# Performance work log

Hardware: AMD Instinct MI355X
Metric: run time of the kernel (lower is better)

Reference implementation:

```python
import jax, jax.numpy as jnp
from jax import lax
import numpy as np

EMBED_HD = 3
DECODE_HD = 128
B, TX, TS = 256, 512, 512


def _lstm(x_seq, h0, c0, Wih, Whh, bih, bhh):
    """PyTorch-convention LSTM over time. x_seq: [T, B, D]; returns final h [B, H].
    Gate order i, f, g, o; gates = x W_ih^T + h W_hh^T + b_ih + b_hh."""
    b = bih + bhh

    def step(carry, x_t):
        h, c = carry
        gates = x_t @ Wih.T + h @ Whh.T + b  # [B, 4H]
        i, f, g, o = jnp.split(gates, 4, axis=-1)
        c = jax.nn.sigmoid(f) * c + jax.nn.sigmoid(i) * jnp.tanh(g)
        h = jax.nn.sigmoid(o) * jnp.tanh(c)
        return (h, c), None

    (hT, _cT), _ = lax.scan(step, (h0, c0), x_seq)
    return hT


def setup_inputs() -> dict:
    key = jax.random.key(0)
    ks = jax.random.split(key, 16)
    f32 = jnp.float32
    return {
        "x": jax.random.normal(ks[0], (B, TX, 8), f32),
        "s": jax.random.normal(ks[1], (B, TS, 6), f32),
        "h0": jax.random.normal(ks[2], (B, EMBED_HD), f32),
        "c0": jax.random.normal(ks[3], (B, EMBED_HD), f32),
        "We_ih": jax.random.normal(ks[4], (4 * EMBED_HD, 8), f32) * 0.1,
        "We_hh": jax.random.normal(ks[5], (4 * EMBED_HD, EMBED_HD), f32) * 0.1,
        "be_ih": jax.random.normal(ks[6], (4 * EMBED_HD,), f32) * 0.1,
        "be_hh": jax.random.normal(ks[7], (4 * EMBED_HD,), f32) * 0.1,
        "Wfc_e": jax.random.normal(ks[8], (1, EMBED_HD), f32) * 0.1,
        "bfc_e": jax.random.normal(ks[9], (1,), f32) * 0.1,
        "Wd_ih": jax.random.normal(ks[10], (4 * DECODE_HD, 7), f32) * 0.1,
        "Wd_hh": jax.random.normal(ks[11], (4 * DECODE_HD, DECODE_HD), f32) * 0.1,
        "bd_ih": jax.random.normal(ks[12], (4 * DECODE_HD,), f32) * 0.1,
        "bd_hh": jax.random.normal(ks[13], (4 * DECODE_HD,), f32) * 0.1,
        "Wfc_d": jax.random.normal(ks[14], (2, 6), f32) * 0.1,
        "bfc_d": jax.random.normal(ks[15], (2,), f32) * 0.1,
    }


def reference(x, s, h0, c0, We_ih, We_hh, be_ih, be_hh, Wfc_e, bfc_e,
              Wd_ih, Wd_hh, bd_ih, bd_hh, Wfc_d, bfc_d):
    # ---- encoder: LSTM over x, random initial hidden (h0, c0), take final out ----
    h_enc = _lstm(jnp.swapaxes(x, 0, 1), h0, c0, We_ih, We_hh, be_ih, be_hh)  # [B, 3]
    z = h_enc @ Wfc_e.T + bfc_e  # [B, 1]

    # ---- decoder: LSTM over cat(s_t, z), zero initial hidden ----
    z_seq = jnp.broadcast_to(z[:, None, :], (s.shape[0], s.shape[1], 1))
    s_plus_z = jnp.concatenate([s, z_seq], axis=-1)  # [B, T, 7]
    hz = jnp.zeros((s.shape[0], DECODE_HD), s.dtype)
    h_dec = _lstm(jnp.swapaxes(s_plus_z, 0, 1), hz, hz, Wd_ih, Wd_hh, bd_ih, bd_hh)

    # per the source, decode_fc is applied to s itself (not the LSTM output)
    traj_hat = s @ Wfc_d.T + bfc_d  # [B, T, 2]
    return z, traj_hat, h_dec
```

## Files before the change

### kernel.cpp

```cpp
#include <hip/hip_runtime.h>
#include <math.h>

#define BATCH 256
#define TX 512
#define TS 512
#define DH 128

typedef _Float16 h2 __attribute__((ext_vector_type(2)));

__device__ __forceinline__ float sigf(float x) {
    return __builtin_amdgcn_rcpf(1.0f + __expf(-x));
}
__device__ __forceinline__ float tanhfast(float x) {
    return fmaf(-2.0f, __builtin_amdgcn_rcpf(__expf(2.0f * x) + 1.0f), 1.0f);
}
template<int CTRL>
__device__ __forceinline__ float dpp_f32(float x) {
    return __int_as_float(__builtin_amdgcn_update_dpp(
        0, __float_as_int(x), CTRL, 0xF, 0xF, true));
}
#define DPP_XOR1 0xB1
#define DPP_XOR2 0x4E
#define DPP_BC0  0x00
#define DPP_BC1  0x55
#define DPP_BC2  0xAA

__global__ __launch_bounds__(512) void fused_kernel(
    const float* __restrict__ x, const float* __restrict__ s,
    const float* __restrict__ h0, const float* __restrict__ c0,
    const float* __restrict__ We_ih, const float* __restrict__ We_hh,
    const float* __restrict__ be_ih, const float* __restrict__ be_hh,
    const float* __restrict__ Wfc_e, const float* __restrict__ bfc_e,
    const float* __restrict__ Wd_ih, const float* __restrict__ Wd_hh,
    const float* __restrict__ bd_ih, const float* __restrict__ bd_hh,
    const float* __restrict__ Wfc_d, const float* __restrict__ bfc_d,
    float* __restrict__ out_z, float* __restrict__ out_traj,
    float* __restrict__ out_h)
{
    __shared__ __align__(16) float pre_lds[TX][12];
    __shared__ int hbuf[2][64];
    __shared__ float zslot;

    const int b   = blockIdx.x;
    const int tid = threadIdx.x;
    const int j   = tid >> 2;
    const int q   = tid & 3;

    {
        const float* xp = x + ((size_t)b * TX + tid) * 8;
        const float4 x0 = *(const float4*)(xp);
        const float4 x1 = *(const float4*)(xp + 4);
        float o[12];
        #pragma unroll
        for (int g = 0; g < 4; ++g) {
            #pragma unroll
            for (int kk = 0; kk < 3; ++kk) {
                const int row = g * 3 + kk;
                const float* wr = We_ih + row * 8;
                float d = be_ih[row] + be_hh[row];
                d = fmaf(wr[0], x0.x, d); d = fmaf(wr[1], x0.y, d);
                d = fmaf(wr[2], x0.z, d); d = fmaf(wr[3], x0.w, d);
                d = fmaf(wr[4], x1.x, d); d = fmaf(wr[5], x1.y, d);
                d = fmaf(wr[6], x1.z, d); d = fmaf(wr[7], x1.w, d);
                o[kk * 4 + g] = d;
            }
        }
        float* op = pre_lds[tid];
        *(float4*)(op)     = make_float4(o[0], o[1], o[2],  o[3]);
        *(float4*)(op + 4) = make_float4(o[4], o[5], o[6],  o[7]);
        *(float4*)(op + 8) = make_float4(o[8], o[9], o[10], o[11]);
    }
    if (tid < 64) hbuf[0][tid] = 0;

    {
        const float* st = s + ((size_t)b * TS + tid) * 6;
        const float2 sa = *(const float2*)(st);
        const float2 sbb = *(const float2*)(st + 2);
        const float2 sc = *(const float2*)(st + 4);
        float o0 = bfc_d[0];
        o0 = fmaf(sa.x,  Wfc_d[0], o0); o0 = fmaf(sa.y,  Wfc_d[1], o0);
        o0 = fmaf(sbb.x, Wfc_d[2], o0); o0 = fmaf(sbb.y, Wfc_d[3], o0);
        o0 = fmaf(sc.x,  Wfc_d[4], o0); o0 = fmaf(sc.y,  Wfc_d[5], o0);
        float o1 = bfc_d[1];
        o1 = fmaf(sa.x,  Wfc_d[6],  o1); o1 = fmaf(sa.y,  Wfc_d[7],  o1);
        o1 = fmaf(sbb.x, Wfc_d[8],  o1); o1 = fmaf(sbb.y, Wfc_d[9],  o1);
        o1 = fmaf(sc.x,  Wfc_d[10], o1); o1 = fmaf(sc.y,  Wfc_d[11], o1);
        *(float2*)(out_traj + ((size_t)b * TS + tid) * 2) = make_float2(o0, o1);
    }

    h2 w[4][16];
    #pragma unroll
    for (int g = 0; g < 4; ++g) {
        const float* wp = Wd_hh + (size_t)(g * DH + j) * DH + q * 32;
        #pragma unroll
        for (int k = 0; k < 16; ++k)
            w[g][k] = h2{(_Float16)wp[2 * k], (_Float16)wp[2 * k + 1]};
    }
    const float* wi = Wd_ih + (size_t)(q * DH + j) * 7;
    const float wx0 = wi[0], wx1 = wi[1], wx2 = wi[2];
    const float wx3 = wi[3], wx4 = wi[4], wx5 = wi[5];
    const float bsum = bd_ih[q * DH + j] + bd_hh[q * DH + j];
    const float wz = wi[6];

    __syncthreads();

    if (tid < 4) {
        const int kk = (tid < 3) ? tid : 0;
        float wh[4][3];
        #pragma unroll
        for (int g = 0; g < 4; ++g) {
            const int row = g * 3 + kk;
            #pragma unroll
            for (int n = 0; n < 3; ++n) wh[g][n] = We_hh[row * 3 + n];
        }
        float hv0 = h0[b * 3 + 0], hv1 = h0[b * 3 + 1], hv2 = h0[b * 3 + 2];
        float c = c0[b * 3 + kk];

        float4 P = *(const float4*)(&pre_lds[0][kk * 4]);
        for (int t = 0; t < TX; ++t) {
            const int tn = (t + 1 < TX) ? t + 1 : t;
            const float4 Pn = *(const float4*)(&pre_lds[tn][kk * 4]);

            float a0 = P.x, a1 = P.y, a2 = P.z, a3 = P.w;
            a0 = fmaf(wh[0][0], hv0, a0); a0 = fmaf(wh[0][1], hv1, a0); a0 = fmaf(wh[0][2], hv2, a0);
            a1 = fmaf(wh[1][0], hv0, a1); a1 = fmaf(wh[1][1], hv1, a1); a1 = fmaf(wh[1][2], hv2, a1);
            a2 = fmaf(wh[2][0], hv0, a2); a2 = fmaf(wh[2][1], hv1, a2); a2 = fmaf(wh[2][2], hv2, a2);
            a3 = fmaf(wh[3][0], hv0, a3); a3 = fmaf(wh[3][1], hv1, a3); a3 = fmaf(wh[3][2], hv2, a3);

            const float ig = sigf(a0);
            const float fg = sigf(a1);
            const float gg = tanhfast(a2);
            const float og = sigf(a3);
            c = fmaf(fg, c, ig * gg);
            const float hk = og * tanhfast(c);
            hv0 = dpp_f32<DPP_BC0>(hk);
            hv1 = dpp_f32<DPP_BC1>(hk);
            hv2 = dpp_f32<DPP_BC2>(hk);
            P = Pn;
        }
        if (tid == 0) {
            float zz = bfc_e[0];
            zz = fmaf(hv0, Wfc_e[0], zz);
            zz = fmaf(hv1, Wfc_e[1], zz);
            zz = fmaf(hv2, Wfc_e[2], zz);
            zslot = zz;
            out_z[b] = zz;
        }
    }
    __syncthreads();

    const float gb = bsum + zslot * wz;

    float c = 0.0f;
    float hn = 0.0f;

    const float* sb = s + (size_t)b * TS * 6;
    float2 sA = *(const float2*)(sb);
    float2 sB = *(const float2*)(sb + 2);
    float2 sC = *(const float2*)(sb + 4);
    float2 sD = *(const float2*)(sb + 6);
    float2 sE = *(const float2*)(sb + 8);
    float2 sF = *(const float2*)(sb + 10);

#define DEC_STEP(BUF, XA, XB, XC)                                              \
    {                                                                          \
        const int4* hb = (const int4*)(&hbuf[BUF][q * 16]);                    \
        const int4 hA = hb[0], hB = hb[1], hC = hb[2], hD = hb[3];             \
        float sdot = gb;                                                       \
        sdot = fmaf(wx0, XA.x, sdot);                                          \
        sdot = fmaf(wx1, XA.y, sdot);                                          \
        sdot = fmaf(wx2, XB.x, sdot);                                          \
        sdot = fmaf(wx3, XB.y, sdot);                                          \
        sdot = fmaf(wx4, XC.x, sdot);                                          \
        sdot = fmaf(wx5, XC.y, sdot);                                          \
        h2 hh[16];                                                             \
        hh[0]  = __builtin_bit_cast(h2, hA.x); hh[1]  = __builtin_bit_cast(h2, hA.y); \
        hh[2]  = __builtin_bit_cast(h2, hA.z); hh[3]  = __builtin_bit_cast(h2, hA.w); \
        hh[4]  = __builtin_bit_cast(h2, hB.x); hh[5]  = __builtin_bit_cast(h2, hB.y); \
        hh[6]  = __builtin_bit_cast(h2, hB.z); hh[7]  = __builtin_bit_cast(h2, hB.w); \
        hh[8]  = __builtin_bit_cast(h2, hC.x); hh[9]  = __builtin_bit_cast(h2, hC.y); \
        hh[10] = __builtin_bit_cast(h2, hC.z); hh[11] = __builtin_bit_cast(h2, hC.w); \
        hh[12] = __builtin_bit_cast(h2, hD.x); hh[13] = __builtin_bit_cast(h2, hD.y); \
        hh[14] = __builtin_bit_cast(h2, hD.z); hh[15] = __builtin_bit_cast(h2, hD.w); \
        float acc[4];                                                          \
        _Pragma("unroll")                                                      \
        for (int g = 0; g < 4; ++g) {                                          \
            float p = (g == q) ? sdot : 0.0f;                                  \
            _Pragma("unroll")                                                  \
            for (int k = 0; k < 16; ++k)                                       \
                p = __builtin_amdgcn_fdot2(w[g][k], hh[k], p, false);          \
            acc[g] = p;                                                        \
        }                                                                      \
        _Pragma("unroll")                                                      \
        for (int g = 0; g < 4; ++g) {                                          \
            float v = acc[g];                                                  \
            v += dpp_f32<DPP_XOR1>(v);                                         \
            v += dpp_f32<DPP_XOR2>(v);                                         \
            acc[g] = v;                                                        \
        }                                                                      \
        const float ig = sigf(acc[0]);                                         \
        const float fg = sigf(acc[1]);                                         \
        const float gg = tanhfast(acc[2]);                                     \
        const float og = sigf(acc[3]);                                         \
        c  = fmaf(fg, c, ig * gg);                                             \
        hn = og * tanhfast(c);                                                 \
        if (q == 0) ((_Float16*)hbuf[BUF ^ 1])[j] = (_Float16)hn;              \
        __syncthreads();                                                       \
    }

    for (int t = 0; t < TS; t += 2) {
        DEC_STEP(0, sA, sB, sC);
        {
            const int tn = (t + 2 < TS) ? t + 2 : TS - 1;
            const float* p = sb + (size_t)tn * 6;
            sA = *(const float2*)(p);
            sB = *(const float2*)(p + 2);
            sC = *(const float2*)(p + 4);
        }
        DEC_STEP(1, sD, sE, sF);
        {
            const int tn = (t + 3 < TS) ? t + 3 : TS - 1;
            const float* p = sb + (size_t)tn * 6;
            sD = *(const float2*)(p);
            sE = *(const float2*)(p + 2);
            sF = *(const float2*)(p + 4);
        }
    }
#undef DEC_STEP

    if (q == 0) out_h[(size_t)b * DH + j] = hn;
}

extern "C" void kernel_launch(void* const* d_in, const int* in_sizes, int n_in,
                              void* d_out, int out_size, void* d_ws, size_t ws_size,
                              hipStream_t stream) {
    const float* x      = (const float*)d_in[0];
    const float* s      = (const float*)d_in[1];
    const float* h0     = (const float*)d_in[2];
    const float* c0     = (const float*)d_in[3];
    const float* We_ih  = (const float*)d_in[4];
    const float* We_hh  = (const float*)d_in[5];
    const float* be_ih  = (const float*)d_in[6];
    const float* be_hh  = (const float*)d_in[7];
    const float* Wfc_e  = (const float*)d_in[8];
    const float* bfc_e  = (const float*)d_in[9];
    const float* Wd_ih  = (const float*)d_in[10];
    const float* Wd_hh  = (const float*)d_in[11];
    const float* bd_ih  = (const float*)d_in[12];
    const float* bd_hh  = (const float*)d_in[13];
    const float* Wfc_d  = (const float*)d_in[14];
    const float* bfc_d  = (const float*)d_in[15];

    float* out      = (float*)d_out;
    float* out_z    = out;
    float* out_traj = out + BATCH;
    float* out_h    = out + BATCH + BATCH * TS * 2;

    fused_kernel<<<BATCH, 512, 0, stream>>>(
        x, s, h0, c0, We_ih, We_hh, be_ih, be_hh, Wfc_e, bfc_e,
        Wd_ih, Wd_hh, bd_ih, bd_hh, Wfc_d, bfc_d,
        out_z, out_traj, out_h);
}
```

Before: 452.6 us.

## Halve decoder block to 256 threads with two threads per hidden unit

Reorganizes the decoder recurrence so each hidden unit is split across 2 lanes instead of 4, each lane holding 64-wide fp16 weight slices for all four gates. This drops one DPP reduction stage per gate and halves the number of waves synchronizing at each step's barrier. In exchange each lane does twice as many fdot2 ops per step and holds twice as many weight registers (128 h2 values), which may raise register pressure or cause spills. The prologue loops are adjusted to cover 512 timesteps with 256 threads.

```diff
diff --git a/kernel.cpp b/kernel.cpp
--- a/kernel.cpp
+++ b/kernel.cpp
@@ -20,12 +20,11 @@
         0, __float_as_int(x), CTRL, 0xF, 0xF, true));
 }
 #define DPP_XOR1 0xB1
-#define DPP_XOR2 0x4E
 #define DPP_BC0  0x00
 #define DPP_BC1  0x55
 #define DPP_BC2  0xAA
 
-__global__ __launch_bounds__(512) void fused_kernel(
+__global__ __launch_bounds__(256) void fused_kernel(
     const float* __restrict__ x, const float* __restrict__ s,
     const float* __restrict__ h0, const float* __restrict__ c0,
     const float* __restrict__ We_ih, const float* __restrict__ We_hh,
@@ -43,11 +42,13 @@
 
     const int b   = blockIdx.x;
     const int tid = threadIdx.x;
-    const int j   = tid >> 2;
-    const int q   = tid & 3;
-
-    {
-        const float* xp = x + ((size_t)b * TX + tid) * 8;
+    const int j   = tid >> 1;
+    const int q   = tid & 1;
+
+    #pragma unroll
+    for (int it = 0; it < 2; ++it) {
+        const int t = tid + it * 256;
+        const float* xp = x + ((size_t)b * TX + t) * 8;
         const float4 x0 = *(const float4*)(xp);
         const float4 x1 = *(const float4*)(xp + 4);
         float o[12];
@@ -65,15 +66,17 @@
                 o[kk * 4 + g] = d;
             }
         }
-        float* op = pre_lds[tid];
+        float* op = pre_lds[t];
         *(float4*)(op)     = make_float4(o[0], o[1], o[2],  o[3]);
         *(float4*)(op + 4) = make_float4(o[4], o[5], o[6],  o[7]);
         *(float4*)(op + 8) = make_float4(o[8], o[9], o[10], o[11]);
     }
     if (tid < 64) hbuf[0][tid] = 0;
 
-    {
-        const float* st = s + ((size_t)b * TS + tid) * 6;
+    #pragma unroll
+    for (int it = 0; it < 2; ++it) {
+        const int t = tid + it * 256;
+        const float* st = s + ((size_t)b * TS + t) * 6;
         const float2 sa = *(const float2*)(st);
         const float2 sbb = *(const float2*)(st + 2);
         const float2 sc = *(const float2*)(st + 4);
@@ -85,22 +88,26 @@
         o1 = fmaf(sa.x,  Wfc_d[6],  o1); o1 = fmaf(sa.y,  Wfc_d[7],  o1);
         o1 = fmaf(sbb.x, Wfc_d[8],  o1); o1 = fmaf(sbb.y, Wfc_d[9],  o1);
         o1 = fmaf(sc.x,  Wfc_d[10], o1); o1 = fmaf(sc.y,  Wfc_d[11], o1);
-        *(float2*)(out_traj + ((size_t)b * TS + tid) * 2) = make_float2(o0, o1);
-    }
-
-    h2 w[4][16];
+        *(float2*)(out_traj + ((size_t)b * TS + t) * 2) = make_float2(o0, o1);
+    }
+
+    h2 w[4][32];
     #pragma unroll
     for (int g = 0; g < 4; ++g) {
-        const float* wp = Wd_hh + (size_t)(g * DH + j) * DH + q * 32;
+        const float* wp = Wd_hh + (size_t)(g * DH + j) * DH + q * 64;
         #pragma unroll
-        for (int k = 0; k < 16; ++k)
+        for (int k = 0; k < 32; ++k)
             w[g][k] = h2{(_Float16)wp[2 * k], (_Float16)wp[2 * k + 1]};
     }
-    const float* wi = Wd_ih + (size_t)(q * DH + j) * 7;
-    const float wx0 = wi[0], wx1 = wi[1], wx2 = wi[2];
-    const float wx3 = wi[3], wx4 = wi[4], wx5 = wi[5];
-    const float bsum = bd_ih[q * DH + j] + bd_hh[q * DH + j];
-    const float wz = wi[6];
+    const float* wiA = Wd_ih + (size_t)(q * DH + j) * 7;
+    const float* wiB = Wd_ih + (size_t)((q + 2) * DH + j) * 7;
+    const float wxA0 = wiA[0], wxA1 = wiA[1], wxA2 = wiA[2];
+    const float wxA3 = wiA[3], wxA4 = wiA[4], wxA5 = wiA[5];
+    const float wxB0 = wiB[0], wxB1 = wiB[1], wxB2 = wiB[2];
+    const float wxB3 = wiB[3], wxB4 = wiB[4], wxB5 = wiB[5];
+    const float bsumA = bd_ih[q * DH + j] + bd_hh[q * DH + j];
+    const float bsumB = bd_ih[(q + 2) * DH + j] + bd_hh[(q + 2) * DH + j];
+    const float wzA = wiA[6], wzB = wiB[6];
 
     __syncthreads();
 
@@ -149,7 +156,9 @@
     }
     __syncthreads();
 
-    const float gb = bsum + zslot * wz;
+    const float zv = zslot;
+    const float gbA = bsumA + zv * wzA;
+    const float gbB = bsumB + zv * wzB;
 
     float c = 0.0f;
     float hn = 0.0f;
@@ -164,40 +173,50 @@
 
 #define DEC_STEP(BUF, XA, XB, XC)                                              \
     {                                                                          \
-        const int4* hb = (const int4*)(&hbuf[BUF][q * 16]);                    \
-        const int4 hA = hb[0], hB = hb[1], hC = hb[2], hD = hb[3];             \
-        float sdot = gb;                                                       \
-        sdot = fmaf(wx0, XA.x, sdot);                                          \
-        sdot = fmaf(wx1, XA.y, sdot);                                          \
-        sdot = fmaf(wx2, XB.x, sdot);                                          \
-        sdot = fmaf(wx3, XB.y, sdot);                                          \
-        sdot = fmaf(wx4, XC.x, sdot);                                          \
-        sdot = fmaf(wx5, XC.y, sdot);                                          \
-        h2 hh[16];                                                             \
-        hh[0]  = __builtin_bit_cast(h2, hA.x); hh[1]  = __builtin_bit_cast(h2, hA.y); \
-        hh[2]  = __builtin_bit_cast(h2, hA.z); hh[3]  = __builtin_bit_cast(h2, hA.w); \
-        hh[4]  = __builtin_bit_cast(h2, hB.x); hh[5]  = __builtin_bit_cast(h2, hB.y); \
-        hh[6]  = __builtin_bit_cast(h2, hB.z); hh[7]  = __builtin_bit_cast(h2, hB.w); \
-        hh[8]  = __builtin_bit_cast(h2, hC.x); hh[9]  = __builtin_bit_cast(h2, hC.y); \
-        hh[10] = __builtin_bit_cast(h2, hC.z); hh[11] = __builtin_bit_cast(h2, hC.w); \
-        hh[12] = __builtin_bit_cast(h2, hD.x); hh[13] = __builtin_bit_cast(h2, hD.y); \
-        hh[14] = __builtin_bit_cast(h2, hD.z); hh[15] = __builtin_bit_cast(h2, hD.w); \
+        const int4* hb = (const int4*)(&hbuf[BUF][q * 32]);                    \
+        const int4 H0 = hb[0], H1 = hb[1], H2 = hb[2], H3 = hb[3];             \
+        const int4 H4 = hb[4], H5 = hb[5], H6 = hb[6], H7 = hb[7];             \
+        float sdA = gbA;                                                       \
+        sdA = fmaf(wxA0, XA.x, sdA); sdA = fmaf(wxA1, XA.y, sdA);              \
+        sdA = fmaf(wxA2, XB.x, sdA); sdA = fmaf(wxA3, XB.y, sdA);              \
+        sdA = fmaf(wxA4, XC.x, sdA); sdA = fmaf(wxA5, XC.y, sdA);              \
+        float sdB = gbB;                                                       \
+        sdB = fmaf(wxB0, XA.x, sdB); sdB = fmaf(wxB1, XA.y, sdB);              \
+        sdB = fmaf(wxB2, XB.x, sdB); sdB = fmaf(wxB3, XB.y, sdB);              \
+        sdB = fmaf(wxB4, XC.x, sdB); sdB = fmaf(wxB5, XC.y, sdB);              \
+        h2 hh[32];                                                             \
+        hh[0]  = __builtin_bit_cast(h2, H0.x); hh[1]  = __builtin_bit_cast(h2, H0.y); \
+        hh[2]  = __builtin_bit_cast(h2, H0.z); hh[3]  = __builtin_bit_cast(h2, H0.w); \
+        hh[4]  = __builtin_bit_cast(h2, H1.x); hh[5]  = __builtin_bit_cast(h2, H1.y); \
+        hh[6]  = __builtin_bit_cast(h2, H1.z); hh[7]  = __builtin_bit_cast(h2, H1.w); \
+        hh[8]  = __builtin_bit_cast(h2, H2.x); hh[9]  = __builtin_bit_cast(h2, H2.y); \
+        hh[10] = __builtin_bit_cast(h2, H2.z); hh[11] = __builtin_bit_cast(h2, H2.w); \
+        hh[12] = __builtin_bit_cast(h2, H3.x); hh[13] = __builtin_bit_cast(h2, H3.y); \
+        hh[14] = __builtin_bit_cast(h2, H3.z); hh[15] = __builtin_bit_cast(h2, H3.w); \
+        hh[16] = __builtin_bit_cast(h2, H4.x); hh[17] = __builtin_bit_cast(h2, H4.y); \
+        hh[18] = __builtin_bit_cast(h2, H4.z); hh[19] = __builtin_bit_cast(h2, H4.w); \
+        hh[20] = __builtin_bit_cast(h2, H5.x); hh[21] = __builtin_bit_cast(h2, H5.y); \
+        hh[22] = __builtin_bit_cast(h2, H5.z); hh[23] = __builtin_bit_cast(h2, H5.w); \
+        hh[24] = __builtin_bit_cast(h2, H6.x); hh[25] = __builtin_bit_cast(h2, H6.y); \
+        hh[26] = __builtin_bit_cast(h2, H6.z); hh[27] = __builtin_bit_cast(h2, H6.w); \
+        hh[28] = __builtin_bit_cast(h2, H7.x); hh[29] = __builtin_bit_cast(h2, H7.y); \
+        hh[30] = __builtin_bit_cast(h2, H7.z); hh[31] = __builtin_bit_cast(h2, H7.w); \
         float acc[4];                                                          \
+        acc[0] = (q == 0) ? sdA : 0.0f;                                        \
+        acc[1] = (q == 1) ? sdA : 0.0f;                                        \
+        acc[2] = (q == 0) ? sdB : 0.0f;                                        \
+        acc[3] = (q == 1) ? sdB : 0.0f;                                        \
         _Pragma("unroll")                                                      \
         for (int g = 0; g < 4; ++g) {                                          \
-            float p = (g == q) ? sdot : 0.0f;                                  \
+            float p = acc[g];                                                  \
             _Pragma("unroll")                                                  \
-            for (int k = 0; k < 16; ++k)                                       \
+            for (int k = 0; k < 32; ++k)                                       \
                 p = __builtin_amdgcn_fdot2(w[g][k], hh[k], p, false);          \
             acc[g] = p;                                                        \
         }                                                                      \
         _Pragma("unroll")                                                      \
-        for (int g = 0; g < 4; ++g) {                                          \
-            float v = acc[g];                                                  \
-            v += dpp_f32<DPP_XOR1>(v);                                         \
-            v += dpp_f32<DPP_XOR2>(v);                                         \
-            acc[g] = v;                                                        \
-        }                                                                      \
+        for (int g = 0; g < 4; ++g)                                            \
+            acc[g] += dpp_f32<DPP_XOR1>(acc[g]);                               \
         const float ig = sigf(acc[0]);                                         \
         const float fg = sigf(acc[1]);                                         \
         const float gg = tanhfast(acc[2]);                                     \
@@ -256,7 +275,7 @@
     float* out_traj = out + BATCH;
     float* out_h    = out + BATCH + BATCH * TS * 2;
 
-    fused_kernel<<<BATCH, 512, 0, stream>>>(
+    fused_kernel<<<BATCH, 256, 0, stream>>>(
         x, s, h0, c0, We_ih, We_hh, be_ih, be_hh, Wfc_e, bfc_e,
         Wd_ih, Wd_hh, bd_ih, bd_hh, Wfc_d, bfc_d,
         out_z, out_traj, out_h);
```

After: 449.5 us. No clear change (-0.7%).

## Use MFMA matrix cores for decoder recurrent matvec with precomputed input gates

Applied to the files above, without the earlier changes.

Replaces the per-thread fdot2 recurrent matvec and DPP cross-lane reductions with 16x16x32 f16 MFMA instructions, holding Wd_hh fragments in registers and broadcasting h as the B operand. Input-projection gate terms are precomputed per 64-step chunk into an LDS table in fp16 and used as the MFMA accumulator init. This shortens the serial per-step dependency chain but wastes most MFMA columns, since h is a single vector, and adds LDS traffic plus extra syncs per chunk. Storing input gates in fp16 adds some rounding error.

```diff
diff --git a/kernel.cpp b/kernel.cpp
--- a/kernel.cpp
+++ b/kernel.cpp
@@ -6,7 +6,9 @@
 #define TS 512
 #define DH 128
 
-typedef _Float16 h2 __attribute__((ext_vector_type(2)));
+typedef _Float16 f16x8 __attribute__((ext_vector_type(8)));
+typedef _Float16 f16x4 __attribute__((ext_vector_type(4)));
+typedef float f32x4 __attribute__((ext_vector_type(4)));
 
 __device__ __forceinline__ float sigf(float x) {
     return __builtin_amdgcn_rcpf(1.0f + __expf(-x));
@@ -19,8 +21,6 @@
     return __int_as_float(__builtin_amdgcn_update_dpp(
         0, __float_as_int(x), CTRL, 0xF, 0xF, true));
 }
-#define DPP_XOR1 0xB1
-#define DPP_XOR2 0x4E
 #define DPP_BC0  0x00
 #define DPP_BC1  0x55
 #define DPP_BC2  0xAA
@@ -38,13 +38,20 @@
     float* __restrict__ out_h)
 {
     __shared__ __align__(16) float pre_lds[TX][12];
-    __shared__ int hbuf[2][64];
+    __shared__ __align__(16) _Float16 sgate[64][516];
+    __shared__ __align__(16) _Float16 hbuf[2][DH];
+    __shared__ float base_lds[4 * DH];
+    __shared__ float s_stage[64][8];
     __shared__ float zslot;
 
-    const int b   = blockIdx.x;
-    const int tid = threadIdx.x;
-    const int j   = tid >> 2;
-    const int q   = tid & 3;
+    const int b    = blockIdx.x;
+    const int tid  = threadIdx.x;
+    const int w    = tid >> 6;
+    const int l    = tid & 63;
+    const int p    = l >> 4;
+    const int rsel = l & 3;
+    const int jj   = 16 * w + 4 * p + rsel;
+    const bool writer = ((l & 12) == 0);
 
     {
         const float* xp = x + ((size_t)b * TX + tid) * 8;
@@ -70,13 +77,13 @@
         *(float4*)(op + 4) = make_float4(o[4], o[5], o[6],  o[7]);
         *(float4*)(op + 8) = make_float4(o[8], o[9], o[10], o[11]);
     }
-    if (tid < 64) hbuf[0][tid] = 0;
+    if (tid < DH) hbuf[0][tid] = (_Float16)0.0f;
 
     {
         const float* st = s + ((size_t)b * TS + tid) * 6;
-        const float2 sa = *(const float2*)(st);
+        const float2 sa  = *(const float2*)(st);
         const float2 sbb = *(const float2*)(st + 2);
-        const float2 sc = *(const float2*)(st + 4);
+        const float2 sc  = *(const float2*)(st + 4);
         float o0 = bfc_d[0];
         o0 = fmaf(sa.x,  Wfc_d[0], o0); o0 = fmaf(sa.y,  Wfc_d[1], o0);
         o0 = fmaf(sbb.x, Wfc_d[2], o0); o0 = fmaf(sbb.y, Wfc_d[3], o0);
@@ -88,19 +95,23 @@
         *(float2*)(out_traj + ((size_t)b * TS + tid) * 2) = make_float2(o0, o1);
     }
 
-    h2 w[4][16];
+    f16x8 Afrag[4][4];
     #pragma unroll
     for (int g = 0; g < 4; ++g) {
-        const float* wp = Wd_hh + (size_t)(g * DH + j) * DH + q * 32;
         #pragma unroll
-        for (int k = 0; k < 16; ++k)
-            w[g][k] = h2{(_Float16)wp[2 * k], (_Float16)wp[2 * k + 1]};
-    }
-    const float* wi = Wd_ih + (size_t)(q * DH + j) * 7;
-    const float wx0 = wi[0], wx1 = wi[1], wx2 = wi[2];
-    const float wx3 = wi[3], wx4 = wi[4], wx5 = wi[5];
-    const float bsum = bd_ih[q * DH + j] + bd_hh[q * DH + j];
-    const float wz = wi[6];
+        for (int kt = 0; kt < 4; ++kt) {
+            const float* wp = Wd_hh + (size_t)(g * DH + 16 * w + (l & 15)) * DH
+                              + kt * 32 + p * 8;
+            const float4 lo = *(const float4*)(wp);
+            const float4 hi = *(const float4*)(wp + 4);
+            f16x8 a;
+            a[0] = (_Float16)lo.x; a[1] = (_Float16)lo.y;
+            a[2] = (_Float16)lo.z; a[3] = (_Float16)lo.w;
+            a[4] = (_Float16)hi.x; a[5] = (_Float16)hi.y;
+            a[6] = (_Float16)hi.z; a[7] = (_Float16)hi.w;
+            Afrag[g][kt] = a;
+        }
+    }
 
     __syncthreads();
 
@@ -149,86 +160,91 @@
     }
     __syncthreads();
 
-    const float gb = bsum + zslot * wz;
-
-    float c = 0.0f;
-    float hn = 0.0f;
-
-    const float* sb = s + (size_t)b * TS * 6;
-    float2 sA = *(const float2*)(sb);
-    float2 sB = *(const float2*)(sb + 2);
-    float2 sC = *(const float2*)(sb + 4);
-    float2 sD = *(const float2*)(sb + 6);
-    float2 sE = *(const float2*)(sb + 8);
-    float2 sF = *(const float2*)(sb + 10);
-
-#define DEC_STEP(BUF, XA, XB, XC)                                              \
-    {                                                                          \
-        const int4* hb = (const int4*)(&hbuf[BUF][q * 16]);                    \
-        const int4 hA = hb[0], hB = hb[1], hC = hb[2], hD = hb[3];             \
-        float sdot = gb;                                                       \
-        sdot = fmaf(wx0, XA.x, sdot);                                          \
-        sdot = fmaf(wx1, XA.y, sdot);                                          \
-        sdot = fmaf(wx2, XB.x, sdot);                                          \
-        sdot = fmaf(wx3, XB.y, sdot);                                          \
-        sdot = fmaf(wx4, XC.x, sdot);                                          \
-        sdot = fmaf(wx5, XC.y, sdot);                                          \
-        h2 hh[16];                                                             \
-        hh[0]  = __builtin_bit_cast(h2, hA.x); hh[1]  = __builtin_bit_cast(h2, hA.y); \
-        hh[2]  = __builtin_bit_cast(h2, hA.z); hh[3]  = __builtin_bit_cast(h2, hA.w); \
-        hh[4]  = __builtin_bit_cast(h2, hB.x); hh[5]  = __builtin_bit_cast(h2, hB.y); \
-        hh[6]  = __builtin_bit_cast(h2, hB.z); hh[7]  = __builtin_bit_cast(h2, hB.w); \
-        hh[8]  = __builtin_bit_cast(h2, hC.x); hh[9]  = __builtin_bit_cast(h2, hC.y); \
-        hh[10] = __builtin_bit_cast(h2, hC.z); hh[11] = __builtin_bit_cast(h2, hC.w); \
-        hh[12] = __builtin_bit_cast(h2, hD.x); hh[13] = __builtin_bit_cast(h2, hD.y); \
-        hh[14] = __builtin_bit_cast(h2, hD.z); hh[15] = __builtin_bit_cast(h2, hD.w); \
-        float acc[4];                                                          \
-        _Pragma("unroll")                                                      \
-        for (int g = 0; g < 4; ++g) {                                          \
-            float p = (g == q) ? sdot : 0.0f;                                  \
-            _Pragma("unroll")                                                  \
-            for (int k = 0; k < 16; ++k)                                       \
-                p = __builtin_amdgcn_fdot2(w[g][k], hh[k], p, false);          \
-            acc[g] = p;                                                        \
-        }                                                                      \
-        _Pragma("unroll")                                                      \
-        for (int g = 0; g < 4; ++g) {                                          \
-            float v = acc[g];                                                  \
-            v += dpp_f32<DPP_XOR1>(v);                                         \
-            v += dpp_f32<DPP_XOR2>(v);                                         \
-            acc[g] = v;                                                        \
-        }                                                                      \
-        const float ig = sigf(acc[0]);                                         \
-        const float fg = sigf(acc[1]);                                         \
-        const float gg = tanhfast(acc[2]);                                     \
-        const float og = sigf(acc[3]);                                         \
-        c  = fmaf(fg, c, ig * gg);                                             \
-        hn = og * tanhfast(c);                                                 \
-        if (q == 0) ((_Float16*)hbuf[BUF ^ 1])[j] = (_Float16)hn;              \
-        __syncthreads();                                                       \
-    }
-
-    for (int t = 0; t < TS; t += 2) {
-        DEC_STEP(0, sA, sB, sC);
+    base_lds[tid] = bd_ih[tid] + bd_hh[tid] + zslot * Wd_ih[(size_t)tid * 7 + 6];
+
+    float c = 0.0f, hn = 0.0f;
+    const int row_r = 64 * w + l;
+    const float* wi = Wd_ih + (size_t)row_r * 7;
+    const float rw0 = wi[0], rw1 = wi[1], rw2 = wi[2];
+    const float rw3 = wi[3], rw4 = wi[4], rw5 = wi[5];
+
+    for (int chunk = 0; chunk < TS / 64; ++chunk) {
         {
-            const int tn = (t + 2 < TS) ? t + 2 : TS - 1;
-            const float* p = sb + (size_t)tn * 6;
-            sA = *(const float2*)(p);
-            sB = *(const float2*)(p + 2);
-            sC = *(const float2*)(p + 4);
-        }
-        DEC_STEP(1, sD, sE, sF);
+            const int tl = tid >> 3, e = tid & 7;
+            if (e < 6)
+                s_stage[tl][e] = s[((size_t)b * TS + chunk * 64 + tl) * 6 + e];
+        }
+        __syncthreads();
         {
-            const int tn = (t + 3 < TS) ? t + 3 : TS - 1;
-            const float* p = sb + (size_t)tn * 6;
-            sD = *(const float2*)(p);
-            sE = *(const float2*)(p + 2);
-            sF = *(const float2*)(p + 4);
-        }
-    }
-#undef DEC_STEP
-
-    if (q == 0) out_h[(size_t)b * DH + j] = hn;
+            const float bs = base_lds[row_r];
+            for (int tl = 0; tl < 64; ++tl) {
+                float a = bs;
+                a = fmaf(rw0, s_stage[tl][0], a);
+                a = fmaf(rw1, s_stage[tl][1], a);
+                a = fmaf(rw2, s_stage[tl][2], a);
+                a = fmaf(rw3, s_stage[tl][3], a);
+                a = fmaf(rw4, s_stage[tl][4], a);
+                a = fmaf(rw5, s_stage[tl][5], a);
+                sgate[tl][row_r] = (_Float16)a;
+            }
+        }
+        __syncthreads();
+
+        for (int tl = 0; tl < 64; ++tl) {
+            const int t   = chunk * 64 + tl;
+            const int cur = t & 1;
+
+            const f16x8* hb = (const f16x8*)(&hbuf[cur][0]);
+            const f16x8 B0 = hb[p];
+            const f16x8 B1 = hb[4 + p];
+            const f16x8 B2 = hb[8 + p];
+            const f16x8 B3 = hb[12 + p];
+
+            const _Float16* sgp = &sgate[tl][16 * w + 4 * p];
+            const f16x4 s0 = *(const f16x4*)(sgp);
+            const f16x4 s1 = *(const f16x4*)(sgp + DH);
+            const f16x4 s2 = *(const f16x4*)(sgp + 2 * DH);
+            const f16x4 s3 = *(const f16x4*)(sgp + 3 * DH);
+            f32x4 C0 = {(float)s0[0], (float)s0[1], (float)s0[2], (float)s0[3]};
+            f32x4 C1 = {(float)s1[0], (float)s1[1], (float)s1[2], (float)s1[3]};
+            f32x4 C2 = {(float)s2[0], (float)s2[1], (float)s2[2], (float)s2[3]};
+            f32x4 C3 = {(float)s3[0], (float)s3[1], (float)s3[2], (float)s3[3]};
+
+            C0 = __builtin_amdgcn_mfma_f32_16x16x32_f16(Afrag[0][0], B0, C0, 0, 0, 0);
+            C1 = __builtin_amdgcn_mfma_f32_16x16x32_f16(Afrag[1][0], B0, C1, 0, 0, 0);
+            C2 = __builtin_amdgcn_mfma_f32_16x16x32_f16(Afrag[2][0], B0, C2, 0, 0, 0);
+            C3 = __builtin_amdgcn_mfma_f32_16x16x32_f16(Afrag[3][0], B0, C3, 0, 0, 0);
+            C0 = __builtin_amdgcn_mfma_f32_16x16x32_f16(Afrag[0][1], B1, C0, 0, 0, 0);
+            C1 = __builtin_amdgcn_mfma_f32_16x16x32_f16(Afrag[1][1], B1, C1, 0, 0, 0);
+            C2 = __builtin_amdgcn_mfma_f32_16x16x32_f16(Afrag[2][1], B1, C2, 0, 0, 0);
+            C3 = __builtin_amdgcn_mfma_f32_16x16x32_f16(Afrag[3][1], B1, C3, 0, 0, 0);
+            C0 = __builtin_amdgcn_mfma_f32_16x16x32_f16(Afrag[0][2], B2, C0, 0, 0, 0);
+            C1 = __builtin_amdgcn_mfma_f32_16x16x32_f16(Afrag[1][2], B2, C1, 0, 0, 0);
+            C2 = __builtin_amdgcn_mfma_f32_16x16x32_f16(Afrag[2][2], B2, C2, 0, 0, 0);
+            C3 = __builtin_amdgcn_mfma_f32_16x16x32_f16(Afrag[3][2], B2, C3, 0, 0, 0);
+            C0 = __builtin_amdgcn_mfma_f32_16x16x32_f16(Afrag[0][3], B3, C0, 0, 0, 0);
+            C1 = __builtin_amdgcn_mfma_f32_16x16x32_f16(Afrag[1][3], B3, C1, 0, 0, 0);
+            C2 = __builtin_amdgcn_mfma_f32_16x16x32_f16(Afrag[2][3], B3, C2, 0, 0, 0);
+            C3 = __builtin_amdgcn_mfma_f32_16x16x32_f16(Afrag[3][3], B3, C3, 0, 0, 0);
+
+            const float pi = rsel == 0 ? C0[0] : rsel == 1 ? C0[1] : rsel == 2 ? C0[2] : C0[3];
+            const float pf = rsel == 0 ? C1[0] : rsel == 1 ? C1[1] : rsel == 2 ? C1[2] : C1[3];
+            const float pg = rsel == 0 ? C2[0] : rsel == 1 ? C2[1] : rsel == 2 ? C2[2] : C2[3];
+            const float po = rsel == 0 ? C3[0] : rsel == 1 ? C3[1] : rsel == 2 ? C3[2] : C3[3];
+
+            const float ig = sigf(pi);
+            const float fg = sigf(pf);
+            const float gg = tanhfast(pg);
+            const float og = sigf(po);
+            c  = fmaf(fg, c, ig * gg);
+            hn = og * tanhfast(c);
+
+            if (writer) hbuf[cur ^ 1][jj] = (_Float16)hn;
+            __syncthreads();
+        }
+    }
+
+    if (writer) out_h[(size_t)b * DH + jj] = hn;
 }
 
 extern "C" void kernel_launch(void* const* d_in, const int* in_sizes, int n_in,
```

Measured after the change: 495.9 us. 9.6% more time.
